# Performance work log

Hardware: AMD Instinct MI355X
Metric: run time of the kernel (lower is better)

Reference implementation:

```python
import jax, jax.numpy as jnp
import numpy as np
from jax import lax

B, D, H, W = 1, 8, 64, 64
C, WS, NH = 192, 8, 6
N = WS ** 3          # 512 tokens per window
HD = C // NH         # 32
CONV_SCALE = 0.01
EPS = 1e-5
DN = ('NCDHW', 'OIDHW', 'NCDHW')


def _make_rpi():
    c = np.stack(np.meshgrid(np.arange(WS), np.arange(WS), np.arange(WS), indexing='ij')).reshape(3, -1)
    rel = (c[:, :, None] - c[:, None, :]).transpose(1, 2, 0) + (WS - 1)  # [N,N,3]
    idx = rel[..., 0] * (2 * WS - 1) ** 2 + rel[..., 1] * (2 * WS - 1) + rel[..., 2]
    return jnp.asarray(idx, dtype=jnp.int32)


def _ln(x, g, b):
    m = x.mean(-1, keepdims=True)
    v = jnp.mean((x - m) ** 2, -1, keepdims=True)
    return (x - m) * lax.rsqrt(v + EPS) * g + b


def setup_inputs() -> dict:
    key = jax.random.key(0)
    ks = jax.random.split(key, 16)
    s = 0.02
    inp = {
        'x': jax.random.normal(ks[0], (B, D * H * W, C), jnp.float32),
        'norm1_g': jnp.ones((C,), jnp.float32), 'norm1_b': jnp.zeros((C,), jnp.float32),
        'qkv_w': jax.random.normal(ks[1], (3 * C, C), jnp.float32) * s,
        'qkv_b': jnp.zeros((3 * C,), jnp.float32),
        'rpb_table': jax.random.normal(ks[2], (3375, NH), jnp.float32) * s,
        'proj_w': jax.random.normal(ks[3], (C, C), jnp.float32) * s,
        'proj_b': jnp.zeros((C,), jnp.float32),
        'conv1_w': jax.random.normal(ks[4], (C // 3, C, 3, 3, 3), jnp.float32) * s,
        'conv1_b': jnp.zeros((C // 3,), jnp.float32),
        'conv2_w': jax.random.normal(ks[5], (C, C // 3, 3, 3, 3), jnp.float32) * s,
        'conv2_b': jnp.zeros((C,), jnp.float32),
        'ca1_w': jax.random.normal(ks[6], (6, C), jnp.float32) * s,
        'ca1_b': jnp.zeros((6,), jnp.float32),
        'ca2_w': jax.random.normal(ks[7], (C, 6), jnp.float32) * s,
        'ca2_b': jnp.zeros((C,), jnp.float32),
        'norm2_g': jnp.ones((C,), jnp.float32), 'norm2_b': jnp.zeros((C,), jnp.float32),
        'fc1_w': jax.random.normal(ks[8], (4 * C, C), jnp.float32) * s,
        'fc1_b': jnp.zeros((4 * C,), jnp.float32),
        'fc2_w': jax.random.normal(ks[9], (C, 4 * C), jnp.float32) * s,
        'fc2_b': jnp.zeros((C,), jnp.float32),
        'rpi': _make_rpi(),
    }
    return inp


def reference(x, norm1_g, norm1_b, qkv_w, qkv_b, rpb_table, proj_w, proj_b,
              conv1_w, conv1_b, conv2_w, conv2_b, ca1_w, ca1_b, ca2_w, ca2_b,
              norm2_g, norm2_b, fc1_w, fc1_b, fc2_w, fc2_b, rpi):
    shortcut = x
    xn = _ln(x, norm1_g, norm1_b)                      # [B, L, C]
    x5 = xn.reshape(B, D, H, W, C)

    # ---- CAB3D conv branch (conv3x3 -> gelu -> conv3x3 -> channel attention)
    xc = jnp.transpose(x5, (0, 4, 1, 2, 3))            # NCDHW
    h = lax.conv_general_dilated(xc, conv1_w, (1, 1, 1), 'SAME', dimension_numbers=DN)
    h = jax.nn.gelu(h + conv1_b[None, :, None, None, None], approximate=False)
    h = lax.conv_general_dilated(h, conv2_w, (1, 1, 1), 'SAME', dimension_numbers=DN)
    h = h + conv2_b[None, :, None, None, None]
    pooled = h.mean(axis=(2, 3, 4))                    # [B, C] global avg pool
    a = jax.nn.relu(pooled @ ca1_w.T + ca1_b)
    a = jax.nn.sigmoid(a @ ca2_w.T + ca2_b)            # [B, C]
    conv_x = (h * a[:, :, None, None, None])
    conv_x = jnp.transpose(conv_x, (0, 2, 3, 4, 1)).reshape(B, D * H * W, C)

    # ---- window partition (shift_size forced to 0 since min(res)==window_size)
    xw = x5.reshape(B, D // WS, WS, H // WS, WS, W // WS, WS, C)
    xw = jnp.transpose(xw, (0, 1, 3, 5, 2, 4, 6, 7)).reshape(-1, N, C)  # [nW, N, C]

    # ---- window attention with relative position bias
    qkv = (xw @ qkv_w.T + qkv_b).reshape(-1, N, 3, NH, HD)
    q = jnp.transpose(qkv[:, :, 0], (0, 2, 1, 3)) * (HD ** -0.5)  # [nW, h, N, d]
    k = jnp.transpose(qkv[:, :, 1], (0, 2, 1, 3))
    v = jnp.transpose(qkv[:, :, 2], (0, 2, 1, 3))
    attn = jnp.einsum('whnd,whmd->whnm', q, k)
    bias = rpb_table[rpi]                              # [N, N, h]
    attn = attn + jnp.transpose(bias, (2, 0, 1))[None]
    attn = jax.nn.softmax(attn, axis=-1)
    out = jnp.einsum('whnm,whmd->whnd', attn, v)
    out = jnp.transpose(out, (0, 2, 1, 3)).reshape(-1, N, C)
    out = out @ proj_w.T + proj_b

    # ---- window reverse
    out = out.reshape(B, D // WS, H // WS, W // WS, WS, WS, WS, C)
    out = jnp.transpose(out, (0, 1, 4, 2, 5, 3, 6, 7)).reshape(B, D * H * W, C)

    x2 = shortcut + out + conv_x * CONV_SCALE
    xm = _ln(x2, norm2_g, norm2_b)
    xm = jax.nn.gelu(xm @ fc1_w.T + fc1_b, approximate=False) @ fc2_w.T + fc2_b
    return x2 + xm
```

## Files before the change

kernel.cpp:

```cpp
#include <hip/hip_runtime.h>
#include <hip/hip_bf16.h>

#define LTOK  32768
#define CDIM  192
#define DD_   8
#define HH_   64
#define WW_   64
#define NHEAD 6
#define HDIM  32
#define NWIN  64
#define NTOKW 512
#define C3    64
#define FCH   768

#define OFF_XN     0u
#define OFF_QH     6291456u
#define OFF_KH     9437184u
#define OFF_VH     12582912u
#define OFF_Y      15728640u
#define OFF_YBF    18874368u
#define OFF_H1     22020096u
#define OFF_H2     24117248u
#define OFF_PART   30408704u
#define OFF_AMASK  30457856u
#define OFF_BIAST  30458048u
#define OFF_W1T    32030912u
#define OFF_W2T    32362688u
#define OFF_QKVT   32694464u
#define OFF_PROJT  32805056u
#define OFF_FC1T   32841920u
#define OFF_FC2T   32989376u

typedef __attribute__((ext_vector_type(8)))  short short8v;
typedef __attribute__((ext_vector_type(16))) float f32x16;

union FragU { short8v v; unsigned u[4]; };

__device__ __forceinline__ float gelu_exact(float x) {
    return 0.5f * x * (1.0f + erff(x * 0.70710678118654752f));
}

__device__ __forceinline__ unsigned short bf16bits(float x) {
    union { __hip_bfloat16 b; unsigned short u; } cv;
    cv.b = __float2bfloat16(x);
    return cv.u;
}

__global__ __launch_bounds__(256) void k_ln(const float* __restrict__ in,
                                            const float* __restrict__ g,
                                            const float* __restrict__ b,
                                            float* __restrict__ out,
                                            __hip_bfloat16* __restrict__ obf) {
    int wv = threadIdx.x >> 6, lane = threadIdx.x & 63;
    int t = blockIdx.x * 4 + wv;
    const float* row = in + (size_t)t * CDIM;
    float x0 = row[lane], x1 = row[lane + 64], x2 = row[lane + 128];
    float s = x0 + x1 + x2;
    for (int o = 32; o; o >>= 1) s += __shfl_xor(s, o);
    float m = s * (1.0f / 192.0f);
    float d0 = x0 - m, d1 = x1 - m, d2 = x2 - m;
    float vv = d0 * d0 + d1 * d1 + d2 * d2;
    for (int o = 32; o; o >>= 1) vv += __shfl_xor(vv, o);
    float inv = rsqrtf(vv * (1.0f / 192.0f) + 1e-5f);
    size_t base = (size_t)t * CDIM;
    float y0 = d0 * inv * g[lane]       + b[lane];
    float y1 = d1 * inv * g[lane + 64]  + b[lane + 64];
    float y2 = d2 * inv * g[lane + 128] + b[lane + 128];
    if (out) {
        out[base + lane]       = y0;
        out[base + lane + 64]  = y1;
        out[base + lane + 128] = y2;
    }
    if (obf) {
        obf[base + lane]       = __float2bfloat16(y0);
        obf[base + lane + 64]  = __float2bfloat16(y1);
        obf[base + lane + 128] = __float2bfloat16(y2);
    }
}

__global__ void k_cast(const float* __restrict__ in, __hip_bfloat16* __restrict__ out, int n) {
    int i = blockIdx.x * 256 + threadIdx.x;
    if (i < n) out[i] = __float2bfloat16(in[i]);
}

__global__ void k_wp1(const float* __restrict__ w, __hip_bfloat16* __restrict__ wp) {
    int i = blockIdx.x * 256 + threadIdx.x;
    if (i >= 331776) return;
    int j = i & 7, oc = (i >> 3) & 63, h = (i >> 9) & 1;
    int cg = (i >> 10) % 12, kk = i / 12288;
    int c = cg * 16 + h * 8 + j;
    wp[i] = __float2bfloat16(w[((size_t)oc * 192 + c) * 27 + kk]);
}
__global__ void k_wp2(const float* __restrict__ w, __hip_bfloat16* __restrict__ wp) {
    int i = blockIdx.x * 256 + threadIdx.x;
    if (i >= 331776) return;
    int j = i & 7, oc = (i >> 3) % 192;
    int h = (i / 1536) & 1, cg = (i / 3072) & 3, kk = i / 12288;
    int c = cg * 16 + h * 8 + j;
    wp[i] = __float2bfloat16(w[((size_t)oc * 64 + c) * 27 + kk]);
}

__global__ __launch_bounds__(256) void k_bias(const int* __restrict__ rpi,
                                              const float* __restrict__ rpb,
                                              float* __restrict__ biasT) {
    __shared__ int idxl[64][64];
    int tid = threadIdx.x;
    int n0 = (blockIdx.x >> 3) * 64, m0 = (blockIdx.x & 7) * 64;
    for (int it = 0; it < 16; it++) {
        int e = it * 256 + tid;
        int ln_ = e >> 6, lm = e & 63;
        idxl[ln_][lm] = rpi[(size_t)(n0 + ln_) * NTOKW + m0 + lm];
    }
    __syncthreads();
    for (int it = 0; it < 16; it++) {
        int e = it * 256 + tid;
        int lm = e >> 6, ln_ = e & 63;
        int id = idxl[ln_][lm];
        #pragma unroll
        for (int h = 0; h < NHEAD; h++)
            biasT[(size_t)h * NTOKW * NTOKW + (size_t)(m0 + lm) * NTOKW + n0 + ln_] =
                rpb[id * NHEAD + h];
    }
}

__global__ __launch_bounds__(256) void k_conv1m(const __hip_bfloat16* __restrict__ xnbf,
                                                const __hip_bfloat16* __restrict__ w1p,
                                                const float* __restrict__ b1,
                                                __hip_bfloat16* __restrict__ h1bf) {
    __shared__ __align__(16) char lds[66 * 384];
    int tid = threadIdx.x;
    int wv = tid >> 6, lane = tid & 63;
    int wr = wv >> 1, wc = wv & 1;
    int half = lane >> 5, l31 = lane & 31;
    int row = blockIdx.x;
    int d = row >> 6, hh = row & 63;

    if (tid < 48) {
        float4 z = {0.f, 0.f, 0.f, 0.f};
        char* p = lds + ((tid < 24) ? tid * 16 : 65 * 384 + (tid - 24) * 16);
        *(float4*)p = z;
    }

    f32x16 acc;
    #pragma unroll
    for (int r = 0; r < 16; r++) acc[r] = 0.f;

    for (int kd = -1; kd <= 1; kd++) {
        int dd = d + kd;
        if (dd < 0 || dd >= DD_) continue;
        for (int kh = -1; kh <= 1; kh++) {
            int h2 = hh + kh;
            if (h2 < 0 || h2 >= HH_) continue;
            const short* src = (const short*)xnbf + ((size_t)((dd << 12) | (h2 << 6))) * CDIM;
            __syncthreads();
            #pragma unroll
            for (int it = 0; it < 6; it++) {
                int e16 = it * 256 + tid;
                int tok = e16 / 24, cb = (e16 % 24) * 16;
                short8v vdat = *(const short8v*)(src + e16 * 8);
                int lrow = tok + 1;
                *(short8v*)(lds + lrow * 384 + (cb ^ ((lrow & 7) << 4))) = vdat;
            }
            __syncthreads();
            #pragma unroll
            for (int kw = -1; kw <= 1; kw++) {
                int kk = (kd + 1) * 9 + (kh + 1) * 3 + (kw + 1);
                int atok = 32 * wr + l31 + kw + 1;
                int akey = (atok & 7) << 4;
                const char* abase = lds + atok * 384;
                const short* wbase = (const short*)w1p + (kk * 24 + half) * 512 + (32 * wc + l31) * 8;
                #pragma unroll
                for (int cg = 0; cg < 12; cg++) {
                    short8v af = *(const short8v*)(abase + ((cg * 32 + half * 16) ^ akey));
                    short8v bf = *(const short8v*)(wbase + cg * 1024);
                    acc = __builtin_amdgcn_mfma_f32_32x32x16_bf16(af, bf, acc, 0, 0, 0);
                }
            }
        }
    }
    int oc = 32 * wc + l31;
    float bb = b1[oc];
    int t0 = row * 64;
    #pragma unroll
    for (int r = 0; r < 16; r++) {
        int tok = 32 * wr + (r & 3) + 8 * (r >> 2) + 4 * half;
        h1bf[(size_t)(t0 + tok) * C3 + oc] = __float2bfloat16(gelu_exact(acc[r] + bb));
    }
}

__global__ __launch_bounds__(384) void k_conv2m(const __hip_bfloat16* __restrict__ h1bf,
                                                const __hip_bfloat16* __restrict__ w2p,
                                                const float* __restrict__ b2,
                                                float* __restrict__ h2) {
    __shared__ __align__(16) char lds[34 * 128];
    int tid = threadIdx.x;
    int wv = tid >> 6, lane = tid & 63;
    int half = lane >> 5, l31 = lane & 31;
    int row = blockIdx.x >> 1, hr = blockIdx.x & 1;
    int d = row >> 6, hh = row & 63;

    f32x16 acc;
    #pragma unroll
    for (int r = 0; r < 16; r++) acc[r] = 0.f;

    for (int kd = -1; kd <= 1; kd++) {
        int dd = d + kd;
        if (dd < 0 || dd >= DD_) continue;
        for (int kh = -1; kh <= 1; kh++) {
            int h2r = hh + kh;
            if (h2r < 0 || h2r >= HH_) continue;
            __syncthreads();
            if (tid < 272) {
                int ti = tid >> 3, cb = (tid & 7) * 16;
                int w = hr * 32 + ti - 1;
                short8v vdat = {0, 0, 0, 0, 0, 0, 0, 0};
                if (w >= 0 && w < 64)
                    vdat = *(const short8v*)((const short*)h1bf +
                           (size_t)((dd << 12) | (h2r << 6) | w) * C3 + cb / 2);
                *(short8v*)(lds + ti * 128 + (cb ^ ((ti & 7) << 4))) = vdat;
            }
            __syncthreads();
            #pragma unroll
            for (int kw = -1; kw <= 1; kw++) {
                int kk = (kd + 1) * 9 + (kh + 1) * 3 + (kw + 1);
                int atok = l31 + kw + 1;
                int akey = (atok & 7) << 4;
                const char* abase = lds + atok * 128;
                const short* wbase = (const short*)w2p + (kk * 8 + half) * 1536 + (wv * 32 + l31) * 8;
                #pragma unroll
                for (int cg = 0; cg < 4; cg++) {
                    short8v af = *(const short8v*)(abase + ((cg * 32 + half * 16) ^ akey));
                    short8v bf = *(const short8v*)(wbase + cg * 3072);
                    acc = __builtin_amdgcn_mfma_f32_32x32x16_bf16(af, bf, acc, 0, 0, 0);
                }
            }
        }
    }
    int oc = wv * 32 + l31;
    float bb = b2[oc];
    int t0 = row * 64 + hr * 32;
    #pragma unroll
    for (int r = 0; r < 16; r++) {
        int tok = (r & 3) + 8 * (r >> 2) + 4 * half;
        h2[(size_t)(t0 + tok) * CDIM + oc] = acc[r] + bb;
    }
}

__global__ __launch_bounds__(192) void k_pool(const float* __restrict__ h2,
                                              float* __restrict__ part) {
    int c = threadIdx.x, b = blockIdx.x;
    float s = 0.f;
    for (int i = 0; i < 128; i++) s += h2[(size_t)(b * 128 + i) * CDIM + c];
    part[b * CDIM + c] = s;
}

__global__ __launch_bounds__(192) void k_ca(const float* __restrict__ part,
                                            const float* __restrict__ ca1w,
                                            const float* __restrict__ ca1b,
                                            const float* __restrict__ ca2w,
                                            const float* __restrict__ ca2b,
                                            float* __restrict__ amask) {
    __shared__ float pooled[CDIM];
    __shared__ float hid[6];
    int c = threadIdx.x;
    float s = 0.f;
    for (int b = 0; b < 256; b++) s += part[b * CDIM + c];
    pooled[c] = s * (1.0f / 32768.0f);
    __syncthreads();
    if (c < 6) {
        float a = ca1b[c];
        for (int j = 0; j < CDIM; j++) a += ca1w[c * CDIM + j] * pooled[j];
        hid[c] = fmaxf(a, 0.f);
    }
    __syncthreads();
    float a = ca2b[c];
    for (int j = 0; j < 6; j++) a += ca2w[c * 6 + j] * hid[j];
    amask[c] = 1.0f / (1.0f + expf(-a));
}

__global__ __launch_bounds__(192) void k_qkvm(const __hip_bfloat16* __restrict__ xnbf,
                                              const __hip_bfloat16* __restrict__ qwb,
                                              const float* __restrict__ qkvb,
                                              __hip_bfloat16* __restrict__ q,
                                              __hip_bfloat16* __restrict__ k,
                                              __hip_bfloat16* __restrict__ v) {
    __shared__ __align__(16) char xlds[32 * 384];
    __shared__ float tb[3][32][33];
    int tid = threadIdx.x;
    int wv = tid >> 6, lane = tid & 63;
    int half = lane >> 5, l31 = lane & 31;
    int t0 = blockIdx.x * 32;
    int wi = t0 >> 9;
    int wh_ = wi >> 3, ww_ = wi & 7;

    #pragma unroll
    for (int it = 0; it < 4; it++) {
        int e16 = it * 192 + tid;
        int tok = e16 / 24, cb = (e16 % 24) * 16;
        int n = (t0 + tok) & 511;
        int nd = n >> 6, nh = (n >> 3) & 7, nw = n & 7;
        int torig = (nd << 12) | ((wh_ * 8 + nh) << 6) | (ww_ * 8 + nw);
        short8v vdat = *(const short8v*)((const short*)xnbf + (size_t)torig * CDIM + (e16 % 24) * 8);
        *(short8v*)(xlds + tok * 384 + (cb ^ ((tok & 7) << 4))) = vdat;
    }
    __syncthreads();

    int akey = (l31 & 7) << 4;
    const char* xbase = xlds + l31 * 384;
    __hip_bfloat16* dstbase = (wv == 0) ? q : (wv == 1 ? k : v);
    float scale = (wv == 0) ? 0.17677669529663687f : 1.0f;

    for (int j = 0; j < 6; j++) {
        int ti = wv * 6 + j;
        f32x16 acc;
        #pragma unroll
        for (int r = 0; r < 16; r++) acc[r] = 0.f;
        const short* wbase = (const short*)qwb + (size_t)(ti * 32 + l31) * CDIM + half * 8;
        #pragma unroll
        for (int cg = 0; cg < 12; cg++) {
            short8v bf = *(const short8v*)(xbase + ((cg * 32 + half * 16) ^ akey));
            short8v af = *(const short8v*)(wbase + cg * 16);
            acc = __builtin_amdgcn_mfma_f32_32x32x16_bf16(af, bf, acc, 0, 0, 0);
        }
        #pragma unroll
        for (int r = 0; r < 16; r++) {
            int dl = (r & 3) + 8 * (r >> 2) + 4 * half;
            tb[wv][l31][dl] = acc[r];
        }
        asm volatile("s_waitcnt lgkmcnt(0)" ::: "memory");
        __builtin_amdgcn_sched_barrier(0);
        int tok = lane >> 1, d0 = (lane & 1) * 16;
        int n = (t0 + tok) & 511;
        __hip_bfloat16* dst = dstbase +
                              ((size_t)((wi * NHEAD + j) * NTOKW + n)) * HDIM + d0;
        const float* bp = qkvb + ti * 32 + d0;
        short8v o0, o1;
        #pragma unroll
        for (int i = 0; i < 8; i++)
            o0[i] = (short)bf16bits((tb[wv][tok][d0 + i] + bp[i]) * scale);
        #pragma unroll
        for (int i = 0; i < 8; i++)
            o1[i] = (short)bf16bits((tb[wv][tok][d0 + 8 + i] + bp[8 + i]) * scale);
        *(short8v*)((short*)dst) = o0;
        *(short8v*)((short*)dst + 8) = o1;
        asm volatile("s_waitcnt lgkmcnt(0)" ::: "memory");
        __builtin_amdgcn_sched_barrier(0);
    }
}

__global__ __launch_bounds__(256) void k_attn(const __hip_bfloat16* __restrict__ qh,
                                              const __hip_bfloat16* __restrict__ kh,
                                              const __hip_bfloat16* __restrict__ vh,
                                              const float* __restrict__ biasT,
                                              __hip_bfloat16* __restrict__ outbf) {
    __shared__ float ot[4][32][33];
    int wv = threadIdx.x >> 6, lane = threadIdx.x & 63;
    int tile = blockIdx.x * 4 + wv;
    int qt = tile & 15, wh = tile >> 4;
    int head = wh % NHEAD, wi = wh / NHEAD;
    int qb = qt * 32;
    int h = lane >> 5, ln31 = lane & 31;

    const unsigned short* qp = (const unsigned short*)qh + ((size_t)wh * NTOKW + qb + ln31) * HDIM;
    short8v qf0 = *(const short8v*)(qp + 8 * h);
    short8v qf1 = *(const short8v*)(qp + 16 + 8 * h);
    const unsigned short* kbase = (const unsigned short*)kh + (size_t)wh * NTOKW * HDIM;
    const unsigned short* vbase = (const unsigned short*)vh + (size_t)wh * NTOKW * HDIM;
    const float* bbase = biasT + (size_t)head * NTOKW * NTOKW + qb + ln31;

    f32x16 O;
    #pragma unroll
    for (int r = 0; r < 16; r++) O[r] = 0.f;
    float m = -1e30f, l = 0.f;

    for (int kb = 0; kb < NTOKW; kb += 32) {
        const unsigned short* kp = kbase + (size_t)(kb + ln31) * HDIM;
        short8v kf0 = *(const short8v*)(kp + 8 * h);
        short8v kf1 = *(const short8v*)(kp + 16 + 8 * h);
        f32x16 S;
        #pragma unroll
        for (int r = 0; r < 16; r++) S[r] = 0.f;
        S = __builtin_amdgcn_mfma_f32_32x32x16_bf16(kf0, qf0, S, 0, 0, 0);
        S = __builtin_amdgcn_mfma_f32_32x32x16_bf16(kf1, qf1, S, 0, 0, 0);

        float s[16];
        #pragma unroll
        for (int r = 0; r < 16; r++) {
            int key = (r & 3) + 8 * (r >> 2) + 4 * h;
            s[r] = S[r] + bbase[(size_t)(kb + key) * NTOKW];
        }
        float cm = s[0];
        #pragma unroll
        for (int r = 1; r < 16; r++) cm = fmaxf(cm, s[r]);
        cm = fmaxf(cm, __shfl_xor(cm, 32));
        float mn = fmaxf(m, cm);
        float scale = __expf(m - mn);
        float e[16]; float cs = 0.f;
        #pragma unroll
        for (int r = 0; r < 16; r++) { e[r] = __expf(s[r] - mn); cs += e[r]; }
        cs += __shfl_xor(cs, 32);
        l = l * scale + cs;
        m = mn;
        #pragma unroll
        for (int r = 0; r < 16; r++) O[r] *= scale;

        unsigned P[8], Qx[8];
        #pragma unroll
        for (int i = 0; i < 8; i++)
            P[i] = (unsigned)bf16bits(e[2 * i]) | ((unsigned)bf16bits(e[2 * i + 1]) << 16);
        #pragma unroll
        for (int i = 0; i < 8; i++) Qx[i] = __shfl_xor(P[i], 32);

        FragU p0, p1;
        p0.u[0] = h ? Qx[2] : P[0];  p0.u[1] = h ? Qx[3] : P[1];
        p0.u[2] = h ? P[2]  : Qx[0]; p0.u[3] = h ? P[3]  : Qx[1];
        p1.u[0] = h ? Qx[6] : P[4];  p1.u[1] = h ? Qx[7] : P[5];
        p1.u[2] = h ? P[6]  : Qx[4]; p1.u[3] = h ? P[7]  : Qx[5];

        const unsigned short* vp0 = vbase + (size_t)(kb + 8 * h) * HDIM + ln31;
        const unsigned short* vp1 = vbase + (size_t)(kb + 16 + 8 * h) * HDIM + ln31;
        short8v vf0, vf1;
        #pragma unroll
        for (int i = 0; i < 8; i++) {
            vf0[i] = (short)vp0[i * HDIM];
            vf1[i] = (short)vp1[i * HDIM];
        }
        O = __builtin_amdgcn_mfma_f32_32x32x16_bf16(vf0, p0.v, O, 0, 0, 0);
        O = __builtin_amdgcn_mfma_f32_32x32x16_bf16(vf1, p1.v, O, 0, 0, 0);
    }

    float invl = 1.0f / l;
    #pragma unroll
    for (int r = 0; r < 16; r++) {
        int d = (r & 3) + 8 * (r >> 2) + 4 * h;
        ot[wv][ln31][d] = O[r] * invl;
    }
    __syncthreads();
    int t2 = lane >> 1, c0 = (lane & 1) * 16;
    short* outp = (short*)outbf + ((size_t)(wi * NTOKW + qb + t2)) * CDIM + head * HDIM + c0;
    short8v s0, s1;
    #pragma unroll
    for (int i = 0; i < 8; i++) s0[i] = (short)bf16bits(ot[wv][t2][c0 + i]);
    #pragma unroll
    for (int i = 0; i < 8; i++) s1[i] = (short)bf16bits(ot[wv][t2][c0 + 8 + i]);
    *(short8v*)outp = s0;
    *(short8v*)(outp + 8) = s1;
}

__global__ __launch_bounds__(192) void k_projm(const __hip_bfloat16* __restrict__ attnbf,
                                               const __hip_bfloat16* __restrict__ pwb,
                                               const float* __restrict__ pb,
                                               const float* __restrict__ x,
                                               const float* __restrict__ h2,
                                               const float* __restrict__ amask,
                                               float* __restrict__ x2) {
    __shared__ __align__(16) char alds[32 * 384];
    __shared__ float tb[3][32][33];
    int tid = threadIdx.x;
    int wv = tid >> 6, lane = tid & 63;
    int half = lane >> 5, l31 = lane & 31;
    int t0 = blockIdx.x * 32;
    int wi = t0 >> 9;
    int wh_ = wi >> 3, ww_ = wi & 7;

    const short* src = (const short*)attnbf + (size_t)t0 * CDIM;
    #pragma unroll
    for (int it = 0; it < 4; it++) {
        int e16 = it * 192 + tid;
        int tok = e16 / 24, cb = (e16 % 24) * 16;
        short8v vdat = *(const short8v*)(src + e16 * 8);
        *(short8v*)(alds + tok * 384 + (cb ^ ((tok & 7) << 4))) = vdat;
    }
    __syncthreads();

    int akey = (l31 & 7) << 4;
    const char* abase = alds + l31 * 384;

    for (int j = 0; j < 2; j++) {
        int ot = wv * 2 + j;
        f32x16 acc;
        #pragma unroll
        for (int r = 0; r < 16; r++) acc[r] = 0.f;
        const short* wbase = (const short*)pwb + (size_t)(ot * 32 + l31) * CDIM + half * 8;
        #pragma unroll
        for (int cg = 0; cg < 12; cg++) {
            short8v bf = *(const short8v*)(abase + ((cg * 32 + half * 16) ^ akey));
            short8v af = *(const short8v*)(wbase + cg * 16);
            acc = __builtin_amdgcn_mfma_f32_32x32x16_bf16(af, bf, acc, 0, 0, 0);
        }
        #pragma unroll
        for (int r = 0; r < 16; r++) {
            int oc = (r & 3) + 8 * (r >> 2) + 4 * half;
            tb[wv][l31][oc] = acc[r];
        }
        asm volatile("s_waitcnt lgkmcnt(0)" ::: "memory");
        __builtin_amdgcn_sched_barrier(0);
        int tok = lane >> 1, c0 = (lane & 1) * 16;
        int n = (t0 + tok) & 511;
        int nd = n >> 6, nh = (n >> 3) & 7, nw = n & 7;
        int t = (nd << 12) | ((wh_ * 8 + nh) << 6) | (ww_ * 8 + nw);
        size_t idx = (size_t)t * CDIM + ot * 32 + c0;
        const float* bp = pb + ot * 32 + c0;
        const float* ap = amask + ot * 32 + c0;
        #pragma unroll
        for (int i = 0; i < 16; i++)
            x2[idx + i] = x[idx + i] + tb[wv][tok][c0 + i] + bp[i] + 0.01f * h2[idx + i] * ap[i];
        asm volatile("s_waitcnt lgkmcnt(0)" ::: "memory");
        __builtin_amdgcn_sched_barrier(0);
    }
}

__global__ __launch_bounds__(256) void k_mlpm(const __hip_bfloat16* __restrict__ ybf,
                                              const __hip_bfloat16* __restrict__ w1b,
                                              const float* __restrict__ b1,
                                              const __hip_bfloat16* __restrict__ w2b,
                                              const float* __restrict__ b2,
                                              float* __restrict__ out) {
    __shared__ __align__(16) char ylds[32 * 384];
    __shared__ __align__(16) float rbuf[6 * 32 * 32];
    int tid = threadIdx.x;
    int wv = tid >> 6, lane = tid & 63;
    int half = lane >> 5, l31 = lane & 31;
    int t0 = blockIdx.x * 32;

    const short* src = (const short*)ybf + (size_t)t0 * CDIM;
    #pragma unroll
    for (int it = 0; it < 3; it++) {
        int e16 = it * 256 + tid;
        int tok = e16 / 24, cb = (e16 % 24) * 16;
        short8v vdat = *(const short8v*)(src + e16 * 8);
        *(short8v*)(ylds + tok * 384 + (cb ^ ((tok & 7) << 4))) = vdat;
    }
    __syncthreads();

    int akey = (l31 & 7) << 4;
    const char* ybase = ylds + l31 * 384;

    f32x16 oacc[6];
    #pragma unroll
    for (int ot = 0; ot < 6; ot++)
        #pragma unroll
        for (int r = 0; r < 16; r++) oacc[ot][r] = 0.f;

    for (int j = 0; j < 6; j++) {
        int hc = wv * 6 + j;
        f32x16 hacc;
        #pragma unroll
        for (int r = 0; r < 16; r++) hacc[r] = 0.f;
        const short* w1base = (const short*)w1b + (size_t)(hc * 32 + l31) * CDIM + half * 8;
        #pragma unroll
        for (int cg = 0; cg < 12; cg++) {
            short8v bf = *(const short8v*)(ybase + ((cg * 32 + half * 16) ^ akey));
            short8v af = *(const short8v*)(w1base + cg * 16);
            hacc = __builtin_amdgcn_mfma_f32_32x32x16_bf16(af, bf, hacc, 0, 0, 0);
        }
        float e[16];
        #pragma unroll
        for (int r = 0; r < 16; r++) {
            int hid = (r & 3) + 8 * (r >> 2) + 4 * half;
            e[r] = gelu_exact(hacc[r] + b1[hc * 32 + hid]);
        }
        unsigned P[8], Qx[8];
        #pragma unroll
        for (int i = 0; i < 8; i++)
            P[i] = (unsigned)bf16bits(e[2 * i]) | ((unsigned)bf16bits(e[2 * i + 1]) << 16);
        #pragma unroll
        for (int i = 0; i < 8; i++) Qx[i] = __shfl_xor(P[i], 32);
        FragU p0, p1;
        p0.u[0] = half ? Qx[2] : P[0];  p0.u[1] = half ? Qx[3] : P[1];
        p0.u[2] = half ? P[2]  : Qx[0]; p0.u[3] = half ? P[3]  : Qx[1];
        p1.u[0] = half ? Qx[6] : P[4];  p1.u[1] = half ? Qx[7] : P[5];
        p1.u[2] = half ? P[6]  : Qx[4]; p1.u[3] = half ? P[7]  : Qx[5];

        const short* w2base = (const short*)w2b + (size_t)l31 * FCH + hc * 32 + half * 8;
        #pragma unroll
        for (int ot = 0; ot < 6; ot++) {
            short8v a0 = *(const short8v*)(w2base + (size_t)ot * 32 * FCH);
            short8v a1 = *(const short8v*)(w2base + (size_t)ot * 32 * FCH + 16);
            oacc[ot] = __builtin_amdgcn_mfma_f32_32x32x16_bf16(a0, p0.v, oacc[ot], 0, 0, 0);
            oacc[ot] = __builtin_amdgcn_mfma_f32_32x32x16_bf16(a1, p1.v, oacc[ot], 0, 0, 0);
        }
    }

    float4* rb4 = (float4*)rbuf;
    for (int w = 0; w < 4; w++) {
        if (wv == w) {
            #pragma unroll
            for (int ot = 0; ot < 6; ot++) {
                #pragma unroll
                for (int g = 0; g < 4; g++) {
                    float4 val = {oacc[ot][g * 4 + 0], oacc[ot][g * 4 + 1],
                                  oacc[ot][g * 4 + 2], oacc[ot][g * 4 + 3]};
                    int chunk = 2 * g + half;
                    float4* p = &rb4[(ot * 32 + l31) * 8 + (chunk ^ (l31 & 7))];
                    if (w == 0) *p = val;
                    else {
                        float4 o = *p;
                        o.x += val.x; o.y += val.y; o.z += val.z; o.w += val.w;
                        *p = o;
                    }
                }
            }
        }
        __syncthreads();
    }

    #pragma unroll
    for (int i = 0; i < 6; i++) {
        int c4 = i * 256 + tid;
        int oc4 = c4 & 7;
        int tok = (c4 >> 3) & 31;
        int ot  = c4 >> 8;
        float4 vv = rb4[(ot * 32 + tok) * 8 + (oc4 ^ (tok & 7))];
        float* op = out + (size_t)(t0 + tok) * CDIM + ot * 32 + oc4 * 4;
        const float* bp = b2 + ot * 32 + oc4 * 4;
        op[0] += vv.x + bp[0];
        op[1] += vv.y + bp[1];
        op[2] += vv.z + bp[2];
        op[3] += vv.w + bp[3];
    }
}

extern "C" void kernel_launch(void* const* d_in, const int* in_sizes, int n_in,
                              void* d_out, int out_size, void* d_ws, size_t ws_size,
                              hipStream_t stream) {
    const float* x     = (const float*)d_in[0];
    const float* n1g   = (const float*)d_in[1];
    const float* n1b   = (const float*)d_in[2];
    const float* qkvw  = (const float*)d_in[3];
    const float* qkvb  = (const float*)d_in[4];
    const float* rpb   = (const float*)d_in[5];
    const float* projw = (const float*)d_in[6];
    const float* projb = (const float*)d_in[7];
    const float* c1w   = (const float*)d_in[8];
    const float* c1b   = (const float*)d_in[9];
    const float* c2w   = (const float*)d_in[10];
    const float* c2b   = (const float*)d_in[11];
    const float* ca1w  = (const float*)d_in[12];
    const float* ca1b  = (const float*)d_in[13];
    const float* ca2w  = (const float*)d_in[14];
    const float* ca2b  = (const float*)d_in[15];
    const float* n2g   = (const float*)d_in[16];
    const float* n2b   = (const float*)d_in[17];
    const float* fc1w  = (const float*)d_in[18];
    const float* fc1b  = (const float*)d_in[19];
    const float* fc2w  = (const float*)d_in[20];
    const float* fc2b  = (const float*)d_in[21];
    const int*   rpi   = (const int*)d_in[22];

    float* ws  = (float*)d_ws;
    float* out = (float*)d_out;

    __hip_bfloat16* attnbf = (__hip_bfloat16*)(ws + OFF_XN);
    __hip_bfloat16* qh   = (__hip_bfloat16*)(ws + OFF_QH);
    __hip_bfloat16* kb_  = (__hip_bfloat16*)(ws + OFF_KH);
    __hip_bfloat16* vb_  = (__hip_bfloat16*)(ws + OFF_VH);
    __hip_bfloat16* xnbf = (__hip_bfloat16*)(ws + OFF_Y);
    __hip_bfloat16* ybf  = (__hip_bfloat16*)(ws + OFF_YBF);
    __hip_bfloat16* h1bf = (__hip_bfloat16*)(ws + OFF_H1);
    float* h2    = ws + OFF_H2;
    float* part  = ws + OFF_PART;
    float* amask = ws + OFF_AMASK;
    float* biasT = ws + OFF_BIAST;
    __hip_bfloat16* w1p  = (__hip_bfloat16*)(ws + OFF_W1T);
    __hip_bfloat16* w2p  = (__hip_bfloat16*)(ws + OFF_W2T);
    __hip_bfloat16* qwb  = (__hip_bfloat16*)(ws + OFF_QKVT);
    __hip_bfloat16* pwb  = (__hip_bfloat16*)(ws + OFF_PROJT);
    __hip_bfloat16* w1b  = (__hip_bfloat16*)(ws + OFF_FC1T);
    __hip_bfloat16* w2b  = (__hip_bfloat16*)(ws + OFF_FC2T);

    k_wp1<<<(331776 + 255) / 256, 256, 0, stream>>>(c1w, w1p);
    k_wp2<<<(331776 + 255) / 256, 256, 0, stream>>>(c2w, w2p);
    k_cast<<<(110592 + 255) / 256, 256, 0, stream>>>(qkvw, qwb, 110592);
    k_cast<<<(36864 + 255) / 256, 256, 0, stream>>>(projw, pwb, 36864);
    k_cast<<<(147456 + 255) / 256, 256, 0, stream>>>(fc1w, w1b, 147456);
    k_cast<<<(147456 + 255) / 256, 256, 0, stream>>>(fc2w, w2b, 147456);
    k_bias<<<64, 256, 0, stream>>>(rpi, rpb, biasT);

    k_ln<<<LTOK / 4, 256, 0, stream>>>(x, n1g, n1b, (float*)nullptr, xnbf);
    k_conv1m<<<512, 256, 0, stream>>>(xnbf, w1p, c1b, h1bf);
    k_conv2m<<<1024, 384, 0, stream>>>(h1bf, w2p, c2b, h2);
    k_pool<<<256, 192, 0, stream>>>(h2, part);
    k_ca<<<1, 192, 0, stream>>>(part, ca1w, ca1b, ca2w, ca2b, amask);
    k_qkvm<<<LTOK / 32, 192, 0, stream>>>(xnbf, qwb, qkvb, qh, kb_, vb_);
    k_attn<<<(NWIN * NHEAD * 16) / 4, 256, 0, stream>>>(qh, kb_, vb_, biasT, attnbf);
    k_projm<<<LTOK / 32, 192, 0, stream>>>(attnbf, pwb, projb, x, h2, amask, out);
    k_ln<<<LTOK / 4, 256, 0, stream>>>(out, n2g, n2b, (float*)nullptr, ybf);
    k_mlpm<<<LTOK / 32, 256, 0, stream>>>(ybf, w1b, fc1b, w2b, fc2b, out);
}
```

Before: 430.2 us.

## Pre-pack linear weights into MFMA fragment order and split accumulators

Replaces the plain fp32-to-bf16 weight casts with a packing kernel that stores each 32-row by 16-column weight tile in MFMA A-fragment order. Each lane's 16-byte load is then contiguous with its neighbours', so a wave reads a dense 512-byte block instead of strided row segments from global memory. The qkv, proj and fc1 GEMM loops also use two independent accumulators to break the MFMA dependency chain, summing them at the end. This costs extra accumulator registers, which could lower occupancy.

```diff
diff --git a/kernel.cpp b/kernel.cpp
--- a/kernel.cpp
+++ b/kernel.cpp
@@ -78,9 +78,16 @@
     }
 }
 
-__global__ void k_cast(const float* __restrict__ in, __hip_bfloat16* __restrict__ out, int n) {
+__global__ void k_wpack(const float* __restrict__ w, __hip_bfloat16* __restrict__ wp,
+                        int R, int C) {
     int i = blockIdx.x * 256 + threadIdx.x;
-    if (i < n) out[i] = __float2bfloat16(in[i]);
+    if (i >= R * C) return;
+    int j = i & 7, l31 = (i >> 3) & 31, half = (i >> 8) & 1;
+    int rest = i >> 9;
+    int nkc = C >> 4;
+    int kc = rest % nkc, rt = rest / nkc;
+    int row = rt * 32 + l31, col = kc * 16 + half * 8 + j;
+    wp[i] = __float2bfloat16(w[(size_t)row * C + col]);
 }
 
 __global__ void k_wp1(const float* __restrict__ w, __hip_bfloat16* __restrict__ wp) {
@@ -312,20 +319,23 @@
 
     for (int j = 0; j < 6; j++) {
         int ti = wv * 6 + j;
-        f32x16 acc;
-        #pragma unroll
-        for (int r = 0; r < 16; r++) acc[r] = 0.f;
-        const short* wbase = (const short*)qwb + (size_t)(ti * 32 + l31) * CDIM + half * 8;
-        #pragma unroll
-        for (int cg = 0; cg < 12; cg++) {
-            short8v bf = *(const short8v*)(xbase + ((cg * 32 + half * 16) ^ akey));
-            short8v af = *(const short8v*)(wbase + cg * 16);
-            acc = __builtin_amdgcn_mfma_f32_32x32x16_bf16(af, bf, acc, 0, 0, 0);
+        f32x16 a0, a1;
+        #pragma unroll
+        for (int r = 0; r < 16; r++) { a0[r] = 0.f; a1[r] = 0.f; }
+        const short* wbase = (const short*)qwb + ti * 6144 + half * 256 + l31 * 8;
+        #pragma unroll
+        for (int cg = 0; cg < 12; cg += 2) {
+            short8v bf0 = *(const short8v*)(xbase + ((cg * 32 + half * 16) ^ akey));
+            short8v bf1 = *(const short8v*)(xbase + (((cg + 1) * 32 + half * 16) ^ akey));
+            short8v af0 = *(const short8v*)(wbase + cg * 512);
+            short8v af1 = *(const short8v*)(wbase + (cg + 1) * 512);
+            a0 = __builtin_amdgcn_mfma_f32_32x32x16_bf16(af0, bf0, a0, 0, 0, 0);
+            a1 = __builtin_amdgcn_mfma_f32_32x32x16_bf16(af1, bf1, a1, 0, 0, 0);
         }
         #pragma unroll
         for (int r = 0; r < 16; r++) {
             int dl = (r & 3) + 8 * (r >> 2) + 4 * half;
-            tb[wv][l31][dl] = acc[r];
+            tb[wv][l31][dl] = a0[r] + a1[r];
         }
         asm volatile("s_waitcnt lgkmcnt(0)" ::: "memory");
         __builtin_amdgcn_sched_barrier(0);
@@ -478,20 +488,23 @@
 
     for (int j = 0; j < 2; j++) {
         int ot = wv * 2 + j;
-        f32x16 acc;
-        #pragma unroll
-        for (int r = 0; r < 16; r++) acc[r] = 0.f;
-        const short* wbase = (const short*)pwb + (size_t)(ot * 32 + l31) * CDIM + half * 8;
-        #pragma unroll
-        for (int cg = 0; cg < 12; cg++) {
-            short8v bf = *(const short8v*)(abase + ((cg * 32 + half * 16) ^ akey));
-            short8v af = *(const short8v*)(wbase + cg * 16);
-            acc = __builtin_amdgcn_mfma_f32_32x32x16_bf16(af, bf, acc, 0, 0, 0);
+        f32x16 a0, a1;
+        #pragma unroll
+        for (int r = 0; r < 16; r++) { a0[r] = 0.f; a1[r] = 0.f; }
+        const short* wbase = (const short*)pwb + ot * 6144 + half * 256 + l31 * 8;
+        #pragma unroll
+        for (int cg = 0; cg < 12; cg += 2) {
+            short8v bf0 = *(const short8v*)(abase + ((cg * 32 + half * 16) ^ akey));
+            short8v bf1 = *(const short8v*)(abase + (((cg + 1) * 32 + half * 16) ^ akey));
+            short8v af0 = *(const short8v*)(wbase + cg * 512);
+            short8v af1 = *(const short8v*)(wbase + (cg + 1) * 512);
+            a0 = __builtin_amdgcn_mfma_f32_32x32x16_bf16(af0, bf0, a0, 0, 0, 0);
+            a1 = __builtin_amdgcn_mfma_f32_32x32x16_bf16(af1, bf1, a1, 0, 0, 0);
         }
         #pragma unroll
         for (int r = 0; r < 16; r++) {
             int oc = (r & 3) + 8 * (r >> 2) + 4 * half;
-            tb[wv][l31][oc] = acc[r];
+            tb[wv][l31][oc] = a0[r] + a1[r];
         }
         asm volatile("s_waitcnt lgkmcnt(0)" ::: "memory");
         __builtin_amdgcn_sched_barrier(0);
@@ -544,21 +557,24 @@
 
     for (int j = 0; j < 6; j++) {
         int hc = wv * 6 + j;
-        f32x16 hacc;
-        #pragma unroll
-        for (int r = 0; r < 16; r++) hacc[r] = 0.f;
-        const short* w1base = (const short*)w1b + (size_t)(hc * 32 + l31) * CDIM + half * 8;
-        #pragma unroll
-        for (int cg = 0; cg < 12; cg++) {
-            short8v bf = *(const short8v*)(ybase + ((cg * 32 + half * 16) ^ akey));
-            short8v af = *(const short8v*)(w1base + cg * 16);
-            hacc = __builtin_amdgcn_mfma_f32_32x32x16_bf16(af, bf, hacc, 0, 0, 0);
+        f32x16 h0, h1;
+        #pragma unroll
+        for (int r = 0; r < 16; r++) { h0[r] = 0.f; h1[r] = 0.f; }
+        const short* w1base = (const short*)w1b + hc * 6144 + half * 256 + l31 * 8;
+        #pragma unroll
+        for (int cg = 0; cg < 12; cg += 2) {
+            short8v bf0 = *(const short8v*)(ybase + ((cg * 32 + half * 16) ^ akey));
+            short8v bf1 = *(const short8v*)(ybase + (((cg + 1) * 32 + half * 16) ^ akey));
+            short8v af0 = *(const short8v*)(w1base + cg * 512);
+            short8v af1 = *(const short8v*)(w1base + (cg + 1) * 512);
+            h0 = __builtin_amdgcn_mfma_f32_32x32x16_bf16(af0, bf0, h0, 0, 0, 0);
+            h1 = __builtin_amdgcn_mfma_f32_32x32x16_bf16(af1, bf1, h1, 0, 0, 0);
         }
         float e[16];
         #pragma unroll
         for (int r = 0; r < 16; r++) {
             int hid = (r & 3) + 8 * (r >> 2) + 4 * half;
-            e[r] = gelu_exact(hacc[r] + b1[hc * 32 + hid]);
+            e[r] = gelu_exact(h0[r] + h1[r] + b1[hc * 32 + hid]);
         }
         unsigned P[8], Qx[8];
         #pragma unroll
@@ -572,11 +588,11 @@
         p1.u[0] = half ? Qx[6] : P[4];  p1.u[1] = half ? Qx[7] : P[5];
         p1.u[2] = half ? P[6]  : Qx[4]; p1.u[3] = half ? P[7]  : Qx[5];
 
-        const short* w2base = (const short*)w2b + (size_t)l31 * FCH + hc * 32 + half * 8;
+        const short* w2base = (const short*)w2b + hc * 1024 + half * 256 + l31 * 8;
         #pragma unroll
         for (int ot = 0; ot < 6; ot++) {
-            short8v a0 = *(const short8v*)(w2base + (size_t)ot * 32 * FCH);
-            short8v a1 = *(const short8v*)(w2base + (size_t)ot * 32 * FCH + 16);
+            short8v a0 = *(const short8v*)(w2base + ot * 24576);
+            short8v a1 = *(const short8v*)(w2base + ot * 24576 + 512);
             oacc[ot] = __builtin_amdgcn_mfma_f32_32x32x16_bf16(a0, p0.v, oacc[ot], 0, 0, 0);
             oacc[ot] = __builtin_amdgcn_mfma_f32_32x32x16_bf16(a1, p1.v, oacc[ot], 0, 0, 0);
         }
@@ -671,10 +687,10 @@
 
     k_wp1<<<(331776 + 255) / 256, 256, 0, stream>>>(c1w, w1p);
     k_wp2<<<(331776 + 255) / 256, 256, 0, stream>>>(c2w, w2p);
-    k_cast<<<(110592 + 255) / 256, 256, 0, stream>>>(qkvw, qwb, 110592);
-    k_cast<<<(36864 + 255) / 256, 256, 0, stream>>>(projw, pwb, 36864);
-    k_cast<<<(147456 + 255) / 256, 256, 0, stream>>>(fc1w, w1b, 147456);
-    k_cast<<<(147456 + 255) / 256, 256, 0, stream>>>(fc2w, w2b, 147456);
+    k_wpack<<<(110592 + 255) / 256, 256, 0, stream>>>(qkvw, qwb, 576, 192);
+    k_wpack<<<(36864 + 255) / 256, 256, 0, stream>>>(projw, pwb, 192, 192);
+    k_wpack<<<(147456 + 255) / 256, 256, 0, stream>>>(fc1w, w1b, 768, 192);
+    k_wpack<<<(147456 + 255) / 256, 256, 0, stream>>>(fc2w, w2b, 192, 768);
     k_bias<<<64, 256, 0, stream>>>(rpi, rpb, biasT);
 
     k_ln<<<LTOK / 4, 256, 0, stream>>>(x, n1g, n1b, (float*)nullptr, xnbf);
```

Result: faster. 384.3 us (-10.7%).
